# Performance work log

Hardware: AMD Instinct MI355X
Metric: run time of the kernel (lower is better)

## Reference

```python
import jax, jax.numpy as jnp
import numpy as np

N = 100000
E = 1600000
NFEAT = 256
NHIDDEN = 128
NCLASS = 40
NLAYERS = 8
INIT_T = 0.5


def setup_inputs() -> dict:
    key = jax.random.key(0)
    ks = jax.random.split(key, 9)
    x = jax.random.normal(ks[0], (N, NFEAT), dtype=jnp.float32)
    edge_row = jax.random.randint(ks[1], (E,), 0, N, dtype=jnp.int32)
    edge_col = jax.random.randint(ks[2], (E,), 0, N, dtype=jnp.int32)
    # small weights so the Chebyshev recurrence stays numerically tame
    edge_weight = jax.random.uniform(ks[3], (E,), dtype=jnp.float32) * (2.0 / 16.0)
    b1 = 1.0 / np.sqrt(NFEAT)
    fc1_w = jax.random.uniform(ks[4], (NFEAT, NHIDDEN), minval=-b1, maxval=b1, dtype=jnp.float32)
    fc1_b = jax.random.uniform(ks[5], (NHIDDEN,), minval=-b1, maxval=b1, dtype=jnp.float32)
    b2 = 1.0 / np.sqrt(NHIDDEN)
    fc2_w = jax.random.uniform(ks[6], (NHIDDEN, NCLASS), minval=-b2, maxval=b2, dtype=jnp.float32)
    fc2_b = jax.random.uniform(ks[7], (NCLASS,), minval=-b2, maxval=b2, dtype=jnp.float32)
    thetas = jnp.full((NLAYERS,), INIT_T, dtype=jnp.float32)
    return {"x": x, "edge_row": edge_row, "edge_col": edge_col,
            "edge_weight": edge_weight, "fc1_w": fc1_w, "fc1_b": fc1_b,
            "fc2_w": fc2_w, "fc2_b": fc2_b, "thetas": thetas}


def _spmm(edge_row, edge_col, edge_weight, t):
    # out[r] = sum_{e: row[e]=r} w[e] * t[col[e]]   (sparse L @ T)
    msgs = edge_weight[:, None] * t[edge_col]  # [E, H]
    return jax.ops.segment_sum(msgs, edge_row, num_segments=N)


def reference(x, edge_row, edge_col, edge_weight, fc1_w, fc1_b, fc2_w, fc2_b, thetas):
    # eval mode: dropout is identity
    h = jax.nn.relu(x @ fc1_w + fc1_b)  # [N, H]
    # filter 0: T_0 = h, poly = theta_0 * T_0
    t0 = h
    poly = thetas[0] * t0
    # filter 1: T_1 = L @ T_0
    t1 = _spmm(edge_row, edge_col, edge_weight, t0)
    poly = poly + thetas[1] * t1
    # remaining filters, replicating the original prevs-update order exactly
    prev0, prev1 = t0, t1
    for i in range(2, NLAYERS):
        ti = 2.0 * _spmm(edge_row, edge_col, edge_weight, prev0) - prev1
        prev1 = prev0
        prev0 = ti
        poly = poly + thetas[i] * ti
    y = poly @ fc2_w + fc2_b  # [N, nclass]
    return jax.nn.log_softmax(y, axis=1)
```

## Files before the change

kernel.cpp:

```cpp
#include <hip/hip_runtime.h>
#include <hip/hip_bf16.h>


#define NFEAT 256
#define NHID  128
#define NCLS  40
#define ELLS  48

typedef __hip_bfloat16 bf16;
typedef __attribute__((ext_vector_type(8))) short bf16x8;
typedef __attribute__((ext_vector_type(4))) float f32x4;

__device__ inline float2 load2b(const bf16* p) {
    __hip_bfloat162 v = *(const __hip_bfloat162*)p;
    return make_float2(__bfloat162float(v.x), __bfloat162float(v.y));
}
__device__ inline void store2b(bf16* p, float2 v) {
    __hip_bfloat162 o;
    o.x = __float2bfloat16(v.x);
    o.y = __float2bfloat16(v.y);
    *(__hip_bfloat162*)p = o;
}

__global__ void zero_ints(int* __restrict__ p, int n) {
    int i = blockIdx.x * blockDim.x + threadIdx.x;
    if (i < n) p[i] = 0;
}

__global__ void scatter_ell(const int* __restrict__ erow, const int* __restrict__ ecol,
                            const float* __restrict__ ew, int* __restrict__ deg,
                            int2* __restrict__ cw_ell, int E) {
    int e = blockIdx.x * blockDim.x + threadIdx.x;
    if (e < E) {
        int r = erow[e];
        int p = atomicAdd(&deg[r], 1);
        if (p < ELLS)
            cw_ell[(size_t)r * ELLS + p] = make_int2(ecol[e], __float_as_int(ew[e]));
    }
}

__global__ void assign_starts(int* __restrict__ deg, int* __restrict__ counter,
                              int* __restrict__ row_start, int N) {
    int r = blockIdx.x * blockDim.x + threadIdx.x;
    int lane = threadIdx.x & 63;
    int d = (r < N) ? min(deg[r], ELLS) : 0;
    int x = d;
    #pragma unroll
    for (int off = 1; off < 64; off <<= 1) {
        int y = __shfl_up(x, off);
        if (lane >= off) x += y;
    }
    int base = 0;
    if (lane == 63) base = atomicAdd(counter, x);
    base = __shfl(base, 63);
    int start = base + (x - d);
    if (r < N) {
        deg[r] = d;
        row_start[r] = start;
    }
}

__global__ __launch_bounds__(256) void compact_copy(
    const int* __restrict__ deg, const int* __restrict__ row_start,
    const int2* __restrict__ cw_ell, int2* __restrict__ cw, int N) {
    int row = blockIdx.x * 16 + (threadIdx.x >> 4);
    if (row >= N) return;
    int l16 = threadIdx.x & 15;
    int d = deg[row];
    const int2* src = cw_ell + (size_t)row * ELLS;
    int2* dst = cw + row_start[row];
    for (int j = l16; j < d; j += 16) dst[j] = src[j];
}

__global__ void hist_kernel(const int* __restrict__ erow, int* __restrict__ deg, int E) {
    int e = blockIdx.x * blockDim.x + threadIdx.x;
    if (e < E) atomicAdd(&deg[erow[e]], 1);
}

__global__ void assign_starts_cur(int* __restrict__ deg, int* __restrict__ counter,
                                  int* __restrict__ row_start, int* __restrict__ cursor, int N) {
    int r = blockIdx.x * blockDim.x + threadIdx.x;
    int lane = threadIdx.x & 63;
    int d = (r < N) ? deg[r] : 0;
    int x = d;
    #pragma unroll
    for (int off = 1; off < 64; off <<= 1) {
        int y = __shfl_up(x, off);
        if (lane >= off) x += y;
    }
    int base = 0;
    if (lane == 63) base = atomicAdd(counter, x);
    base = __shfl(base, 63);
    int start = base + (x - d);
    if (r < N) {
        row_start[r] = start;
        cursor[r] = start;
    }
}

__global__ void scatter_compact(const int* __restrict__ erow, const int* __restrict__ ecol,
                                const float* __restrict__ ew, int* __restrict__ cursor,
                                int2* __restrict__ cw, int E) {
    int e = blockIdx.x * blockDim.x + threadIdx.x;
    if (e < E) {
        int r = erow[e];
        int p = atomicAdd(&cursor[r], 1);
        cw[p] = make_int2(ecol[e], __float_as_int(ew[e]));
    }
}

__global__ __launch_bounds__(256) void fc1_mfma(
    const float* __restrict__ x, const float* __restrict__ W,
    const float* __restrict__ bias, bf16* __restrict__ t0, int n) {
    __shared__ __align__(16) bf16 As[128 * 40];
    __shared__ __align__(16) bf16 Bs[128 * 40];

    const int tid = threadIdx.x;
    const int wave = tid >> 6;
    const int lane = tid & 63;
    const int quad = lane >> 4;
    const int lm = lane & 15;
    const int block_row = blockIdx.x * 128;

    f32x4 acc[2][8];
    #pragma unroll
    for (int s = 0; s < 2; ++s)
        #pragma unroll
        for (int t = 0; t < 8; ++t)
            acc[s][t] = (f32x4){0.f, 0.f, 0.f, 0.f};

    float bcol[8];
    #pragma unroll
    for (int t = 0; t < 8; ++t) bcol[t] = bias[t * 16 + lm];

    for (int kc = 0; kc < NFEAT; kc += 32) {
        #pragma unroll
        for (int i = 0; i < 4; ++i) {
            int idx = tid + 256 * i;
            int row = idx >> 3;
            int c4 = idx & 7;
            int grow = block_row + row;
            float4 v = make_float4(0.f, 0.f, 0.f, 0.f);
            if (grow < n) v = *(const float4*)&x[(size_t)grow * NFEAT + kc + c4 * 4];
            __hip_bfloat162 lo2, hi2;
            lo2.x = __float2bfloat16(v.x); lo2.y = __float2bfloat16(v.y);
            hi2.x = __float2bfloat16(v.z); hi2.y = __float2bfloat16(v.w);
            *(__hip_bfloat162*)&As[row * 40 + c4 * 4] = lo2;
            *(__hip_bfloat162*)&As[row * 40 + c4 * 4 + 2] = hi2;
        }
        #pragma unroll
        for (int i = 0; i < 4; ++i) {
            int idx = tid + 256 * i;
            int nn = idx & 127;
            int k4 = idx >> 7;
            const float* wp = &W[(size_t)(kc + k4 * 4) * NHID + nn];
            float v0 = wp[0];
            float v1 = wp[NHID];
            float v2 = wp[2 * NHID];
            float v3 = wp[3 * NHID];
            __hip_bfloat162 lo2, hi2;
            lo2.x = __float2bfloat16(v0); lo2.y = __float2bfloat16(v1);
            hi2.x = __float2bfloat16(v2); hi2.y = __float2bfloat16(v3);
            *(__hip_bfloat162*)&Bs[nn * 40 + k4 * 4] = lo2;
            *(__hip_bfloat162*)&Bs[nn * 40 + k4 * 4 + 2] = hi2;
        }
        __syncthreads();

        bf16x8 af0 = *(const bf16x8*)&As[(wave * 32 + lm) * 40 + quad * 8];
        bf16x8 af1 = *(const bf16x8*)&As[(wave * 32 + 16 + lm) * 40 + quad * 8];
        #pragma unroll
        for (int t = 0; t < 8; ++t) {
            bf16x8 bf = *(const bf16x8*)&Bs[(t * 16 + lm) * 40 + quad * 8];
            acc[0][t] = __builtin_amdgcn_mfma_f32_16x16x32_bf16(af0, bf, acc[0][t], 0, 0, 0);
            acc[1][t] = __builtin_amdgcn_mfma_f32_16x16x32_bf16(af1, bf, acc[1][t], 0, 0, 0);
        }
        __syncthreads();
    }

    #pragma unroll
    for (int s = 0; s < 2; ++s) {
        #pragma unroll
        for (int r = 0; r < 4; ++r) {
            int grow = block_row + wave * 32 + s * 16 + quad * 4 + r;
            if (grow >= n) continue;
            bf16* orow = t0 + (size_t)grow * NHID + lm;
            #pragma unroll
            for (int t = 0; t < 8; ++t) {
                float v = fmaxf(acc[s][t][r] + bcol[t], 0.f);
                orow[t * 16] = __float2bfloat16(v);
            }
        }
    }
}

template <bool FIRST, int PMODE>
__global__ __launch_bounds__(256) void spmm_cheb(
    const int* __restrict__ row_start, const int* __restrict__ deg,
    const int2* __restrict__ cw,
    const bf16* __restrict__ tprev, const bf16* __restrict__ tsub,
    bf16* __restrict__ tout, float* __restrict__ poly,
    const float* __restrict__ thetas, int layer, int n) {
    int lane = threadIdx.x & 63;
    int wid = (int)((blockIdx.x * (unsigned)blockDim.x + threadIdx.x) >> 6);
    if (wid >= n) return;
    int start = row_start[wid];
    int d = deg[wid];
    const int2* ep = cw + start;
    const int lo = 2 * lane;

    float2 acc = make_float2(0.f, 0.f);
    int j = 0;
    for (; j + 8 <= d; j += 8) {
        int2 e[8];
        #pragma unroll
        for (int u = 0; u < 8; ++u) e[u] = ep[j + u];
        float2 tv[8];
        #pragma unroll
        for (int u = 0; u < 8; ++u) tv[u] = load2b(tprev + (size_t)e[u].x * NHID + lo);
        #pragma unroll
        for (int u = 0; u < 8; ++u) {
            float w = __int_as_float(e[u].y);
            acc.x = fmaf(w, tv[u].x, acc.x);
            acc.y = fmaf(w, tv[u].y, acc.y);
        }
    }
    for (; j < d; ++j) {
        int2 e = ep[j];
        float w = __int_as_float(e.y);
        float2 tv = load2b(tprev + (size_t)e.x * NHID + lo);
        acc.x = fmaf(w, tv.x, acc.x);
        acc.y = fmaf(w, tv.y, acc.y);
    }

    size_t o = (size_t)wid * NHID + lo;
    float2 res, pv;
    if constexpr (FIRST) {
        res = acc;
    } else {
        pv = load2b(tsub + o);
        res = make_float2(2.f * acc.x - pv.x, 2.f * acc.y - pv.y);
    }
    if constexpr (PMODE != 3) store2b(tout + o, res);

    if constexpr (PMODE == 1) {
        float th0 = thetas[0], th12 = thetas[1] + thetas[2], th3 = thetas[3];
        float2 tpv = load2b(tprev + o);
        float2 p;
        p.x = th0 * pv.x + th12 * tpv.x + th3 * res.x;
        p.y = th0 * pv.y + th12 * tpv.y + th3 * res.y;
        *(float2*)&poly[o] = p;
    } else if constexpr (PMODE == 2 || PMODE == 3) {
        float tha = thetas[layer - 1], thb = thetas[layer];
        float2 tpv = load2b(tprev + o);
        float2 p = *(float2*)&poly[o];
        p.x += tha * tpv.x + thb * res.x;
        p.y += tha * tpv.y + thb * res.y;
        *(float2*)&poly[o] = p;
    }
}

__global__ __launch_bounds__(256) void fc2_softmax(
    const float* __restrict__ poly, const float* __restrict__ w2,
    const float* __restrict__ b2, float* __restrict__ out, int n) {
    int row = blockIdx.x * 256 + threadIdx.x;
    if (row >= n) return;

    float acc[NCLS];
    #pragma unroll
    for (int c = 0; c < NCLS; ++c) acc[c] = b2[c];

    const float* pr = poly + (size_t)row * NHID;
    #pragma unroll 1
    for (int k = 0; k < NHID; k += 4) {
        float4 p = *(const float4*)&pr[k];
        const float* wr = w2 + (size_t)k * NCLS;
        #pragma unroll
        for (int c = 0; c < NCLS; ++c) {
            acc[c] = fmaf(p.x, wr[c], acc[c]);
            acc[c] = fmaf(p.y, wr[NCLS + c], acc[c]);
            acc[c] = fmaf(p.z, wr[2 * NCLS + c], acc[c]);
            acc[c] = fmaf(p.w, wr[3 * NCLS + c], acc[c]);
        }
    }

    float m = acc[0];
    #pragma unroll
    for (int c = 1; c < NCLS; ++c) m = fmaxf(m, acc[c]);
    float s = 0.f;
    #pragma unroll
    for (int c = 0; c < NCLS; ++c) s += __expf(acc[c] - m);
    float lse = m + __logf(s);

    float* orow = out + (size_t)row * NCLS;
    #pragma unroll
    for (int c = 0; c < NCLS; c += 4) {
        float4 v = make_float4(acc[c] - lse, acc[c + 1] - lse,
                               acc[c + 2] - lse, acc[c + 3] - lse);
        *(float4*)&orow[c] = v;
    }
}

static void run_spmm_chain(const float* w2, const float* b2, const float* thetas,
                           float* out, int N,
                           const int* row_start, const int* deg, const int2* cw,
                           float* poly, bf16* tX, bf16* tY, bf16* tZ,
                           hipStream_t stream) {
    int spmm_blocks = (int)(((size_t)N * 64 + 255) / 256);
    spmm_cheb<true, 0><<<spmm_blocks, 256, 0, stream>>>(
        row_start, deg, cw, tX, (const bf16*)nullptr, tY, poly, thetas, 1, N);
    spmm_cheb<false, 1><<<spmm_blocks, 256, 0, stream>>>(
        row_start, deg, cw, tY, tX, tZ, poly, thetas, 3, N);
    spmm_cheb<false, 0><<<spmm_blocks, 256, 0, stream>>>(
        row_start, deg, cw, tZ, tY, tX, poly, thetas, 4, N);
    spmm_cheb<false, 2><<<spmm_blocks, 256, 0, stream>>>(
        row_start, deg, cw, tX, tZ, tY, poly, thetas, 5, N);
    spmm_cheb<false, 0><<<spmm_blocks, 256, 0, stream>>>(
        row_start, deg, cw, tY, tX, tZ, poly, thetas, 6, N);
    spmm_cheb<false, 3><<<spmm_blocks, 256, 0, stream>>>(
        row_start, deg, cw, tZ, tY, (bf16*)nullptr, poly, thetas, 7, N);

    fc2_softmax<<<(N + 255) / 256, 256, 0, stream>>>(poly, w2, b2, out, N);
}

extern "C" void kernel_launch(void* const* d_in, const int* in_sizes, int n_in,
                              void* d_out, int out_size, void* d_ws, size_t ws_size,
                              hipStream_t stream) {
    const float* x      = (const float*)d_in[0];
    const int*   erow   = (const int*)d_in[1];
    const int*   ecol   = (const int*)d_in[2];
    const float* ew     = (const float*)d_in[3];
    const float* w1     = (const float*)d_in[4];
    const float* b1     = (const float*)d_in[5];
    const float* w2     = (const float*)d_in[6];
    const float* b2     = (const float*)d_in[7];
    const float* thetas = (const float*)d_in[8];
    float* out = (float*)d_out;

    const int N = in_sizes[0] / NFEAT;
    const int E = in_sizes[1];

    char* ws = (char*)d_ws;
    size_t off = 0;
    auto alloc = [&](size_t bytes) -> void* {
        off = (off + 255) & ~(size_t)255;
        void* p = ws + off;
        off += bytes;
        return p;
    };

    size_t poly_bytes = (size_t)N * NHID * 4;
    size_t ell_bytes  = (size_t)N * ELLS * 8;
    size_t tail = 3 * ((size_t)N * NHID * 2 + 256) + 4096;
    size_t need_ell = (size_t)(N + 1) * 4 + (size_t)N * 4 + (size_t)E * 8 +
                      (poly_bytes > ell_bytes ? poly_bytes : ell_bytes) + tail + 8192;
    size_t need_fb  = (size_t)(N + 1) * 4 + 2 * (size_t)N * 4 + (size_t)E * 8 +
                      poly_bytes + tail + 8192;

    if (need_ell <= ws_size) {
        int*   deg       = (int*)alloc((size_t)(N + 1) * 4);
        int*   counter   = deg + N;
        int*   row_start = (int*)alloc((size_t)N * 4);
        int2*  cw        = (int2*)alloc((size_t)E * 8);
        float* poly      = (float*)alloc(poly_bytes > ell_bytes ? poly_bytes : ell_bytes);
        int2*  cw_ell    = (int2*)poly;
        bf16*  tX        = (bf16*)alloc((size_t)N * NHID * 2);
        bf16*  tY        = (bf16*)alloc((size_t)N * NHID * 2);
        bf16*  tZ        = (bf16*)alloc((size_t)N * NHID * 2);

        zero_ints<<<(N + 1 + 255) / 256, 256, 0, stream>>>(deg, N + 1);
        scatter_ell<<<(E + 255) / 256, 256, 0, stream>>>(erow, ecol, ew, deg, cw_ell, E);
        assign_starts<<<(N + 255) / 256, 256, 0, stream>>>(deg, counter, row_start, N);
        compact_copy<<<(N + 15) / 16, 256, 0, stream>>>(deg, row_start, cw_ell, cw, N);
        fc1_mfma<<<(N + 127) / 128, 256, 0, stream>>>(x, w1, b1, tX, N);
        run_spmm_chain(w2, b2, thetas, out, N,
                       row_start, deg, cw, poly, tX, tY, tZ, stream);
    } else {
        int*   deg       = (int*)alloc((size_t)(N + 1) * 4);
        int*   counter   = deg + N;
        int*   row_start = (int*)alloc((size_t)N * 4);
        int*   cursor    = (int*)alloc((size_t)N * 4);
        int2*  cw        = (int2*)alloc((size_t)E * 8);
        float* poly      = (float*)alloc(poly_bytes);
        bf16*  tX        = (bf16*)alloc((size_t)N * NHID * 2);
        bf16*  tY        = (bf16*)alloc((size_t)N * NHID * 2);
        bf16*  tZ        = (bf16*)alloc((size_t)N * NHID * 2);

        zero_ints<<<(N + 1 + 255) / 256, 256, 0, stream>>>(deg, N + 1);
        hist_kernel<<<(E + 255) / 256, 256, 0, stream>>>(erow, deg, E);
        assign_starts_cur<<<(N + 255) / 256, 256, 0, stream>>>(deg, counter, row_start, cursor, N);
        scatter_compact<<<(E + 255) / 256, 256, 0, stream>>>(erow, ecol, ew, cursor, cw, E);
        fc1_mfma<<<(N + 127) / 128, 256, 0, stream>>>(x, w1, b1, tX, N);
        run_spmm_chain(w2, b2, thetas, out, N,
                       row_start, deg, cw, poly, tX, tY, tZ, stream);
    }
}
```

Before: 867.4 us.

## Bucket edges by column segment and sweep segments across many rows per wave

During CSR compaction, each row's edges are now sorted into 8 buckets by column range, and the per-bucket counts are packed into a 64-bit word per row. The new SpMM kernel gives each wave 25 rows and walks the column segments in order, gathering every row's edges for one segment before moving to the next. The aim is to keep the gathered feature rows for one column range resident in cache, so that source-row gathers hit L2 more often. In exchange it needs 25 float2 accumulators per lane, which raises register pressure, and rows per wave are serialized, which may reduce memory-level parallelism and occupancy.

New measurement: 1.787 ms. 106% more time.

```diff
diff --git a/kernel.cpp b/kernel.cpp
--- a/kernel.cpp
+++ b/kernel.cpp
@@ -6,10 +6,13 @@
 #define NHID  128
 #define NCLS  40
 #define ELLS  48
+#define NSEG  8
+#define RPW   25
 
 typedef __hip_bfloat16 bf16;
 typedef __attribute__((ext_vector_type(8))) short bf16x8;
 typedef __attribute__((ext_vector_type(4))) float f32x4;
+typedef unsigned long long u64;
 
 __device__ inline float2 load2b(const bf16* p) {
     __hip_bfloat162 v = *(const __hip_bfloat162*)p;
@@ -60,16 +63,42 @@
     }
 }
 
-__global__ __launch_bounds__(256) void compact_copy(
+__global__ __launch_bounds__(256) void compact_seg(
     const int* __restrict__ deg, const int* __restrict__ row_start,
-    const int2* __restrict__ cw_ell, int2* __restrict__ cw, int N) {
-    int row = blockIdx.x * 16 + (threadIdx.x >> 4);
-    if (row >= N) return;
-    int l16 = threadIdx.x & 15;
-    int d = deg[row];
+    const int2* __restrict__ cw_ell, int2* __restrict__ cw,
+    u64* __restrict__ segcnt, int N) {
+    __shared__ int cnt[16][NSEG];
+    __shared__ int cur[16][NSEG];
+    const int g = threadIdx.x >> 4;
+    const int l = threadIdx.x & 15;
+    const int row = blockIdx.x * 16 + g;
+    if (l < NSEG) cnt[g][l] = 0;
+    __syncthreads();
+    int d = (row < N) ? deg[row] : 0;
     const int2* src = cw_ell + (size_t)row * ELLS;
-    int2* dst = cw + row_start[row];
-    for (int j = l16; j < d; j += 16) dst[j] = src[j];
+    int2 e0, e1, e2;
+    int b0 = -1, b1 = -1, b2 = -1;
+    if (l < d)      { e0 = src[l];      b0 = (int)(((long long)e0.x * NSEG) / N); atomicAdd(&cnt[g][b0], 1); }
+    if (l + 16 < d) { e1 = src[l + 16]; b1 = (int)(((long long)e1.x * NSEG) / N); atomicAdd(&cnt[g][b1], 1); }
+    if (l + 32 < d) { e2 = src[l + 32]; b2 = (int)(((long long)e2.x * NSEG) / N); atomicAdd(&cnt[g][b2], 1); }
+    __syncthreads();
+    if (l == 0 && row < N) {
+        u64 packed = 0;
+        int run = 0;
+        #pragma unroll
+        for (int b = 0; b < NSEG; ++b) {
+            int cb = cnt[g][b];
+            packed |= (u64)cb << (8 * b);
+            cur[g][b] = run;
+            run += cb;
+        }
+        segcnt[row] = packed;
+    }
+    __syncthreads();
+    int base = (row < N) ? row_start[row] : 0;
+    if (b0 >= 0) { int s = atomicAdd(&cur[g][b0], 1); cw[base + s] = e0; }
+    if (b1 >= 0) { int s = atomicAdd(&cur[g][b1], 1); cw[base + s] = e1; }
+    if (b2 >= 0) { int s = atomicAdd(&cur[g][b2], 1); cw[base + s] = e2; }
 }
 
 __global__ void hist_kernel(const int* __restrict__ erow, int* __restrict__ deg, int E) {
@@ -194,6 +223,86 @@
 }
 
 template <bool FIRST, int PMODE>
+__global__ __launch_bounds__(256) void spmm_seg(
+    const int* __restrict__ row_start, const u64* __restrict__ segcnt,
+    const int2* __restrict__ cw,
+    const bf16* __restrict__ tprev, const bf16* __restrict__ tsub,
+    bf16* __restrict__ tout, float* __restrict__ poly,
+    const float* __restrict__ thetas, int layer, int n) {
+    const int lane = threadIdx.x & 63;
+    const int wid = (int)((blockIdx.x * (unsigned)blockDim.x + threadIdx.x) >> 6);
+    const int r0 = wid * RPW;
+    if (r0 >= n) return;
+    const int lo = 2 * lane;
+
+    float2 acc[RPW];
+    #pragma unroll
+    for (int i = 0; i < RPW; ++i) acc[i] = make_float2(0.f, 0.f);
+
+    for (int p = 0; p < NSEG; ++p) {
+        const u64 maskp = (p == 0) ? 0ULL : ((1ULL << (8 * p)) - 1);
+        #pragma unroll
+        for (int i = 0; i < RPW; ++i) {
+            int r = r0 + i;
+            if (r >= n) continue;
+            u64 c = segcnt[r];
+            int cnt = (int)((c >> (8 * p)) & 255);
+            int off = row_start[r] + (int)(((c & maskp) * 0x0101010101010101ULL) >> 56);
+            const int2* ep = cw + off;
+            int j = 0;
+            for (; j + 2 <= cnt; j += 2) {
+                int2 ea = ep[j], eb = ep[j + 1];
+                float2 ta = load2b(tprev + (size_t)ea.x * NHID + lo);
+                float2 tb = load2b(tprev + (size_t)eb.x * NHID + lo);
+                float wa = __int_as_float(ea.y), wb = __int_as_float(eb.y);
+                acc[i].x = fmaf(wa, ta.x, acc[i].x);
+                acc[i].y = fmaf(wa, ta.y, acc[i].y);
+                acc[i].x = fmaf(wb, tb.x, acc[i].x);
+                acc[i].y = fmaf(wb, tb.y, acc[i].y);
+            }
+            if (j < cnt) {
+                int2 e = ep[j];
+                float w = __int_as_float(e.y);
+                float2 tv = load2b(tprev + (size_t)e.x * NHID + lo);
+                acc[i].x = fmaf(w, tv.x, acc[i].x);
+                acc[i].y = fmaf(w, tv.y, acc[i].y);
+            }
+        }
+    }
+
+    #pragma unroll
+    for (int i = 0; i < RPW; ++i) {
+        int r = r0 + i;
+        if (r >= n) continue;
+        size_t o = (size_t)r * NHID + lo;
+        float2 res, pv;
+        if constexpr (FIRST) {
+            res = acc[i];
+        } else {
+            pv = load2b(tsub + o);
+            res = make_float2(2.f * acc[i].x - pv.x, 2.f * acc[i].y - pv.y);
+        }
+        if constexpr (PMODE != 3) store2b(tout + o, res);
+
+        if constexpr (PMODE == 1) {
+            float th0 = thetas[0], th12 = thetas[1] + thetas[2], th3 = thetas[3];
+            float2 tpv = load2b(tprev + o);
+            float2 pq;
+            pq.x = th0 * pv.x + th12 * tpv.x + th3 * res.x;
+            pq.y = th0 * pv.y + th12 * tpv.y + th3 * res.y;
+            *(float2*)&poly[o] = pq;
+        } else if constexpr (PMODE == 2 || PMODE == 3) {
+            float tha = thetas[layer - 1], thb = thetas[layer];
+            float2 tpv = load2b(tprev + o);
+            float2 pq = *(float2*)&poly[o];
+            pq.x += tha * tpv.x + thb * res.x;
+            pq.y += tha * tpv.y + thb * res.y;
+            *(float2*)&poly[o] = pq;
+        }
+    }
+}
+
+template <bool FIRST, int PMODE>
 __global__ __launch_bounds__(256) void spmm_cheb(
     const int* __restrict__ row_start, const int* __restrict__ deg,
     const int2* __restrict__ cw,
@@ -300,28 +409,6 @@
     }
 }
 
-static void run_spmm_chain(const float* w2, const float* b2, const float* thetas,
-                           float* out, int N,
-                           const int* row_start, const int* deg, const int2* cw,
-                           float* poly, bf16* tX, bf16* tY, bf16* tZ,
-                           hipStream_t stream) {
-    int spmm_blocks = (int)(((size_t)N * 64 + 255) / 256);
-    spmm_cheb<true, 0><<<spmm_blocks, 256, 0, stream>>>(
-        row_start, deg, cw, tX, (const bf16*)nullptr, tY, poly, thetas, 1, N);
-    spmm_cheb<false, 1><<<spmm_blocks, 256, 0, stream>>>(
-        row_start, deg, cw, tY, tX, tZ, poly, thetas, 3, N);
-    spmm_cheb<false, 0><<<spmm_blocks, 256, 0, stream>>>(
-        row_start, deg, cw, tZ, tY, tX, poly, thetas, 4, N);
-    spmm_cheb<false, 2><<<spmm_blocks, 256, 0, stream>>>(
-        row_start, deg, cw, tX, tZ, tY, poly, thetas, 5, N);
-    spmm_cheb<false, 0><<<spmm_blocks, 256, 0, stream>>>(
-        row_start, deg, cw, tY, tX, tZ, poly, thetas, 6, N);
-    spmm_cheb<false, 3><<<spmm_blocks, 256, 0, stream>>>(
-        row_start, deg, cw, tZ, tY, (bf16*)nullptr, poly, thetas, 7, N);
-
-    fc2_softmax<<<(N + 255) / 256, 256, 0, stream>>>(poly, w2, b2, out, N);
-}
-
 extern "C" void kernel_launch(void* const* d_in, const int* in_sizes, int n_in,
                               void* d_out, int out_size, void* d_ws, size_t ws_size,
                               hipStream_t stream) {
@@ -351,15 +438,17 @@
     size_t poly_bytes = (size_t)N * NHID * 4;
     size_t ell_bytes  = (size_t)N * ELLS * 8;
     size_t tail = 3 * ((size_t)N * NHID * 2 + 256) + 4096;
-    size_t need_ell = (size_t)(N + 1) * 4 + (size_t)N * 4 + (size_t)E * 8 +
+    size_t need_seg = (size_t)(N + 1) * 4 + (size_t)N * 4 + (size_t)N * 8 +
+                      (size_t)E * 8 +
                       (poly_bytes > ell_bytes ? poly_bytes : ell_bytes) + tail + 8192;
     size_t need_fb  = (size_t)(N + 1) * 4 + 2 * (size_t)N * 4 + (size_t)E * 8 +
                       poly_bytes + tail + 8192;
 
-    if (need_ell <= ws_size) {
+    if (need_seg <= ws_size) {
         int*   deg       = (int*)alloc((size_t)(N + 1) * 4);
         int*   counter   = deg + N;
         int*   row_start = (int*)alloc((size_t)N * 4);
+        u64*   segcnt    = (u64*)alloc((size_t)N * 8);
         int2*  cw        = (int2*)alloc((size_t)E * 8);
         float* poly      = (float*)alloc(poly_bytes > ell_bytes ? poly_bytes : ell_bytes);
         int2*  cw_ell    = (int2*)poly;
@@ -370,10 +459,25 @@
         zero_ints<<<(N + 1 + 255) / 256, 256, 0, stream>>>(deg, N + 1);
         scatter_ell<<<(E + 255) / 256, 256, 0, stream>>>(erow, ecol, ew, deg, cw_ell, E);
         assign_starts<<<(N + 255) / 256, 256, 0, stream>>>(deg, counter, row_start, N);
-        compact_copy<<<(N + 15) / 16, 256, 0, stream>>>(deg, row_start, cw_ell, cw, N);
+        compact_seg<<<(N + 15) / 16, 256, 0, stream>>>(deg, row_start, cw_ell, cw, segcnt, N);
         fc1_mfma<<<(N + 127) / 128, 256, 0, stream>>>(x, w1, b1, tX, N);
-        run_spmm_chain(w2, b2, thetas, out, N,
-                       row_start, deg, cw, poly, tX, tY, tZ, stream);
+
+        int waves = (N + RPW - 1) / RPW;
+        int blocks = (waves + 3) / 4;
+        spmm_seg<true, 0><<<blocks, 256, 0, stream>>>(
+            row_start, segcnt, cw, tX, (const bf16*)nullptr, tY, poly, thetas, 1, N);
+        spmm_seg<false, 1><<<blocks, 256, 0, stream>>>(
+            row_start, segcnt, cw, tY, tX, tZ, poly, thetas, 3, N);
+        spmm_seg<false, 0><<<blocks, 256, 0, stream>>>(
+            row_start, segcnt, cw, tZ, tY, tX, poly, thetas, 4, N);
+        spmm_seg<false, 2><<<blocks, 256, 0, stream>>>(
+            row_start, segcnt, cw, tX, tZ, tY, poly, thetas, 5, N);
+        spmm_seg<false, 0><<<blocks, 256, 0, stream>>>(
+            row_start, segcnt, cw, tY, tX, tZ, poly, thetas, 6, N);
+        spmm_seg<false, 3><<<blocks, 256, 0, stream>>>(
+            row_start, segcnt, cw, tZ, tY, (bf16*)nullptr, poly, thetas, 7, N);
+
+        fc2_softmax<<<(N + 255) / 256, 256, 0, stream>>>(poly, w2, b2, out, N);
     } else {
         int*   deg       = (int*)alloc((size_t)(N + 1) * 4);
         int*   counter   = deg + N;
@@ -390,7 +494,21 @@
         assign_starts_cur<<<(N + 255) / 256, 256, 0, stream>>>(deg, counter, row_start, cursor, N);
         scatter_compact<<<(E + 255) / 256, 256, 0, stream>>>(erow, ecol, ew, cursor, cw, E);
         fc1_mfma<<<(N + 127) / 128, 256, 0, stream>>>(x, w1, b1, tX, N);
-        run_spmm_chain(w2, b2, thetas, out, N,
-                       row_start, deg, cw, poly, tX, tY, tZ, stream);
-    }
-}
+
+        int spmm_blocks = (int)(((size_t)N * 64 + 255) / 256);
+        spmm_cheb<true, 0><<<spmm_blocks, 256, 0, stream>>>(
+            row_start, deg, cw, tX, (const bf16*)nullptr, tY, poly, thetas, 1, N);
+        spmm_cheb<false, 1><<<spmm_blocks, 256, 0, stream>>>(
+            row_start, deg, cw, tY, tX, tZ, poly, thetas, 3, N);
+        spmm_cheb<false, 0><<<spmm_blocks, 256, 0, stream>>>(
+            row_start, deg, cw, tZ, tY, tX, poly, thetas, 4, N);
+        spmm_cheb<false, 2><<<spmm_blocks, 256, 0, stream>>>(
+            row_start, deg, cw, tX, tZ, tY, poly, thetas, 5, N);
+        spmm_cheb<false, 0><<<spmm_blocks, 256, 0, stream>>>(
+            row_start, deg, cw, tY, tX, tZ, poly, thetas, 6, N);
+        spmm_cheb<false, 3><<<spmm_blocks, 256, 0, stream>>>(
+            row_start, deg, cw, tZ, tY, (bf16*)nullptr, poly, thetas, 7, N);
+
+        fc2_softmax<<<(N + 255) / 256, 256, 0, stream>>>(poly, w2, b2, out, N);
+    }
+}
```
